# Performance work log

Measured on AMD Instinct MI355X. Metric: run time of the kernel, lower is better.

The kernel has to match this reference:

```python
import jax, jax.numpy as jnp
import numpy as np

N_IN, N_REC, N_OUT = 512, 2048, 128
D_MAX = 4      # delays drawn from [0, D_MAX]; possible_delays = 1..D_MAX
DT = 0.001


@jax.custom_vjp
def spike(v):
    # SpikeFunc.forward: heaviside(v > 0)
    return (v > 0.0).astype(v.dtype)

def _spike_fwd(v):
    return spike(v), v

def _spike_bwd(v, g):
    # SpikeFunc.backward: grad passes through unchanged for v >= 0,
    # scaled by relu(1 + v) for v < 0
    return (g * jnp.where(v < 0.0, jnp.maximum(1.0 + v, 0.0), 1.0),)

spike.defvjp(_spike_fwd, _spike_bwd)


def setup_inputs() -> dict:
    key = jax.random.key(0)
    ks = jax.random.split(key, 6)
    B, T = 64, 250
    x = (jax.random.uniform(ks[0], (B, N_IN, T)) < 0.05).astype(jnp.float32)
    delays = jax.random.randint(ks[1], (N_REC, N_REC), 0, D_MAX + 1, dtype=jnp.int32)

    def kaiming_uniform(k, shape, fan):
        bound = float(np.sqrt(6.0 / fan))
        return jax.random.uniform(k, shape, minval=-bound, maxval=bound, dtype=jnp.float32)

    W_i = kaiming_uniform(ks[2], (N_REC, N_IN), N_REC)            # fan_out mode
    W_r = kaiming_uniform(ks[3], (N_REC, N_REC), N_REC) * 0.05    # scaled for stable dynamics
    W_o = kaiming_uniform(ks[4], (N_OUT, N_REC), N_REC)
    return {
        'input_spike_raster': x,
        'delays': delays,
        'W_i': W_i, 'W_r': W_r, 'W_o': W_o,
        'B_r': jnp.zeros((N_REC,), jnp.float32),
        'B_o': jnp.zeros((N_OUT,), jnp.float32),
        'tau_rec': jnp.full((1,), 0.2, jnp.float32),
        'tau_out': jnp.full((1,), 0.2, jnp.float32),
        'thr_rec': jnp.full((1,), 0.5, jnp.float32),
    }


def reference(input_spike_raster, delays, W_i, W_r, W_o, B_r, B_o, tau_rec, tau_out, thr_rec):
    rec_c = jnp.exp(-DT * 10.0 / tau_rec)   # (1,)
    out_c = jnp.exp(-DT * 10.0 / tau_out)   # (1,)
    d_vals = jnp.arange(1, D_MAX + 1)       # possible (nonzero) delays
    # W_r * delay_mask.T for each delay d -> (D, n_rec, n_rec)
    masks = (delays[None, :, :] == d_vals[:, None, None])
    Wd = W_r[None] * jnp.transpose(masks, (0, 2, 1)).astype(W_r.dtype)

    B, n_in, T = input_spike_raster.shape
    xs = jnp.transpose(input_spike_raster, (2, 0, 1))  # (T, B, n_in)
    buf0 = jnp.zeros((D_MAX, B, N_REC), W_r.dtype)     # buf[k] = spikes at t-1-k

    def step(carry, inp):
        mem_rec, mem_out, buf = carry
        t, x_t = inp
        cur = x_t @ W_i.T + B_r                               # (B, n_rec)
        # delay d contributes only if t > d (matches torch `if t > d`)
        valid = (t > d_vals).astype(cur.dtype)                # (D,)
        cur = cur + jnp.einsum('dbn,dmn->bm', buf * valid[:, None, None], Wd)
        mem_rec = mem_rec * rec_c + cur
        z = spike(mem_rec - thr_rec)
        mem_rec = mem_rec - z * thr_rec
        mem_out = mem_out * out_c + z @ W_o.T + B_o
        buf = jnp.concatenate([z[None], buf[:-1]], axis=0)
        return (mem_rec, mem_out, buf), z

    init = (jnp.zeros((B, N_REC), W_r.dtype), jnp.zeros((B, N_OUT), W_r.dtype), buf0)
    (_, mem_out, _), zs = jax.lax.scan(step, init, (jnp.arange(T), xs))
    # torch returns (mem_pot_out, stack(rec_spikes, dim=2)) -> (B, n_rec, T)
    return mem_out, jnp.transpose(zs, (1, 2, 0))
```

## Files before the change

### kernel.cpp

```cpp
#include <hip/hip_runtime.h>

#define NIN  512
#define NREC 2048
#define NOUT 128
#define BB   64
#define TT   250

#define OFF_WRT  0UL
#define OFF_DP2  16777216UL
#define OFF_WIT  17825792UL
#define OFF_WOT  22020096UL
#define OFF_MASK 23068672UL
#define OFF_G    27164672UL
#define OFF_CNT  28213248UL

__device__ __forceinline__ int decode_delay(int v) {
    if (v >= 0 && v <= 4) return v;
    const float f = __int_as_float(v);
    if (f >= 0.5f && f <= 4.5f) return (int)(f + 0.5f);
    return 0;
}
__device__ __forceinline__ int delay_like(int v) {
    if (v >= 0 && v <= 4) return 1;
    const float f = __int_as_float(v);
    return (f >= 0.5f && f <= 4.5f) ? 1 : 0;
}
__device__ __forceinline__ unsigned lane_rank(unsigned long long m) {
    unsigned r = __builtin_amdgcn_mbcnt_lo((unsigned)m, 0u);
    return __builtin_amdgcn_mbcnt_hi((unsigned)(m >> 32), r);
}

__global__ __launch_bounds__(256) void k_prep(
    const void* __restrict__ c4A, const void* __restrict__ c4B,
    const float* __restrict__ Wi, const float* __restrict__ Wo,
    float* __restrict__ WrT, unsigned* __restrict__ dP2,
    float* __restrict__ WiT, float* __restrict__ WoT)
{
    const int* iA = (const int*)c4A;
    const int* iB = (const int*)c4B;
    int cntA = 0, cntB = 0;
    for (int j = 0; j < 64; ++j) { cntA += delay_like(iA[j]); cntB += delay_like(iB[j]); }
    const int*   dl = (cntA >= cntB) ? iA : iB;
    const float* Wr = (cntA >= cntB) ? (const float*)c4B : (const float*)c4A;

    const int idx = blockIdx.x * 256 + threadIdx.x;
    if (idx < NREC * NREC) {
        const int n = idx >> 11, m = idx & 2047;
        const int d = decode_delay(dl[idx]);
        const float w = Wr[(size_t)m * NREC + n];
        WrT[idx] = (d == 0) ? 0.0f : w;
        if ((m & 15) == 0) {
            unsigned pw = 0;
            for (int j = 0; j < 16; ++j) {
                const int dj = decode_delay(dl[idx + j]);
                const unsigned e = (dj == 0) ? 0u : (unsigned)(dj - 1);
                pw |= e << (2 * j);
            }
            dP2[idx >> 4] = pw;
        }
    }
    if (idx < NIN * NREC) {
        const int i = idx >> 11, m = idx & 2047;
        WiT[idx] = Wi[(size_t)m * NIN + i];
    }
    if (idx < NREC * NOUT) {
        const int n = idx >> 7, o = idx & 127;
        WoT[idx] = Wo[(size_t)o * NREC + n];
    }
}


#define ACCEV(wf, ee) { const int dd = (int)(((ee) >> sh) & 3u);                \
    const double wd = (double)(wf);                                             \
    a0 += (dd == 0) ? wd : 0.0; a1 += (dd == 1) ? wd : 0.0;                     \
    a2 += (dd == 2) ? wd : 0.0; a3 += (dd == 3) ? wd : 0.0; }

#define LD1(nn, W, E) { const unsigned n_ = (nn);                               \
    W = WrT[(n_ << 11) | colu]; E = dP2[(n_ << 7) | c4i]; }

#define LOAD8M(base, P) {                                                       \
    const uint4 sv_ = *reinterpret_cast<const uint4*>(&slist[(base)]);          \
    LD1(sv_.x & 0xffffu, w##P##0, e##P##0) LD1(sv_.x >> 16, w##P##1, e##P##1)   \
    LD1(sv_.y & 0xffffu, w##P##2, e##P##2) LD1(sv_.y >> 16, w##P##3, e##P##3)   \
    LD1(sv_.z & 0xffffu, w##P##4, e##P##4) LD1(sv_.z >> 16, w##P##5, e##P##5)   \
    LD1(sv_.w & 0xffffu, w##P##6, e##P##6) LD1(sv_.w >> 16, w##P##7, e##P##7) }

#define ACCP(P) { ACCEV(w##P##0, e##P##0) ACCEV(w##P##1, e##P##1)               \
    ACCEV(w##P##2, e##P##2) ACCEV(w##P##3, e##P##3)                             \
    ACCEV(w##P##4, e##P##4) ACCEV(w##P##5, e##P##5)                             \
    ACCEV(w##P##6, e##P##6) ACCEV(w##P##7, e##P##7) }

__global__ __launch_bounds__(512) void k_main(
    const float* __restrict__ x,
    const float* __restrict__ WrT,
    const unsigned* __restrict__ dP2,
    const float* __restrict__ WiT,
    const float* __restrict__ Br,
    const float* __restrict__ tau_rec, const float* __restrict__ tau_out,
    const float* __restrict__ thr_rec,
    unsigned* __restrict__ spikeMask, unsigned* __restrict__ cnt,
    double* __restrict__ g)
{
    __shared__ int icnt[8];
    __shared__ __align__(16) unsigned short ilist[NIN];
    __shared__ __align__(16) unsigned short slist[NREC];
    __shared__ int stot_s;

    const int gid = blockIdx.x;
    const int r8  = gid & 7, kk = gid >> 3;
    const int q   = r8 >> 1;
    const int b   = kk * 2 + (r8 & 1);
    const int tid  = threadIdx.x;
    const int w    = tid >> 6;
    const int lane = tid & 63;
    const int col  = q * 512 + tid;
    const unsigned colu = (unsigned)col;
    const unsigned c4i  = colu >> 4;
    const int sh        = (col & 15) * 2;

    const double rec_c = exp(-0.01 / (double)tau_rec[0]);
    const double out_c = exp(-0.01 / (double)tau_out[0]);
    const double thr   = (double)thr_rec[0];
    const double br    = (double)Br[col];
    double mem = 0.0, gacc = 0.0;
    double a0 = 0.0, a1 = 0.0, a2 = 0.0, a3 = 0.0;

    const float* xb = x + (size_t)b * NIN * TT;
    const float* Wc = WiT + col;
    float xv = xb[(size_t)tid * TT];

    for (int t = 0; t < TT; ++t) {
        const bool ihit = (xv != 0.f);
        const unsigned long long im = __ballot(ihit);
        if (lane == 0) icnt[w] = __popcll(im);
        float xvn = 0.f;
        if (t + 1 < TT) xvn = xb[(size_t)tid * TT + (t + 1)];
        __syncthreads();
        int ioffw = 0, itot = 0;
#pragma unroll
        for (int j = 0; j < 8; ++j) { const int c = icnt[j]; if (j < w) ioffw += c; itot += c; }
        if (ihit) ilist[ioffw + lane_rank(im)] = (unsigned short)tid;
        __syncthreads();
        double cin = 0.0;
        {
            int k = 0;
            for (; k + 8 <= itot; k += 8) {
                const uint4 sv = *reinterpret_cast<const uint4*>(&ilist[k]);
                const float v0 = Wc[(sv.x & 0xffffu) << 11];
                const float v1 = Wc[(sv.x >> 16)     << 11];
                const float v2 = Wc[(sv.y & 0xffffu) << 11];
                const float v3 = Wc[(sv.y >> 16)     << 11];
                const float v4 = Wc[(sv.z & 0xffffu) << 11];
                const float v5 = Wc[(sv.z >> 16)     << 11];
                const float v6 = Wc[(sv.w & 0xffffu) << 11];
                const float v7 = Wc[(sv.w >> 16)     << 11];
                cin += (double)v0; cin += (double)v1; cin += (double)v2; cin += (double)v3;
                cin += (double)v4; cin += (double)v5; cin += (double)v6; cin += (double)v7;
            }
            for (; k < itot; ++k) cin += (double)Wc[(unsigned)ilist[k] << 11];
        }
        xv = xvn;

        if (t >= 2) {
            const unsigned* gmp = spikeMask + (size_t)((t - 1) * BB + b) * 64;
            if (tid == 0) {
                while (__hip_atomic_load(&cnt[(t - 1) * BB + b],
                                         __ATOMIC_ACQUIRE, __HIP_MEMORY_SCOPE_AGENT) < 4u)
                    __builtin_amdgcn_s_sleep(1);
            }
            __syncthreads();
            if (tid < 64) {
                const unsigned wv = __hip_atomic_load(&gmp[tid],
                                        __ATOMIC_RELAXED, __HIP_MEMORY_SCOPE_AGENT);
                const int zc = __popc(wv);
                int inc = zc;
#pragma unroll
                for (int s = 1; s < 64; s <<= 1) {
                    const int up = __shfl_up(inc, s, 64);
                    if (lane >= s) inc += up;
                }
                int off = inc - zc;
                if (lane == 63) stot_s = inc;
                unsigned bits = wv;
                while (bits) {
                    const int bp = __ffs(bits) - 1;
                    bits &= bits - 1;
                    slist[off++] = (unsigned short)(tid * 32 + bp);
                }
            }
            __syncthreads();
            const int stot = stot_s;
            int k = 0;
            {
                float wA0, wA1, wA2, wA3, wA4, wA5, wA6, wA7;
                float wB0, wB1, wB2, wB3, wB4, wB5, wB6, wB7;
                float wC0, wC1, wC2, wC3, wC4, wC5, wC6, wC7;
                unsigned eA0, eA1, eA2, eA3, eA4, eA5, eA6, eA7;
                unsigned eB0, eB1, eB2, eB3, eB4, eB5, eB6, eB7;
                unsigned eC0, eC1, eC2, eC3, eC4, eC5, eC6, eC7;
                if (stot >= 48) {
                    LOAD8M(0, A) LOAD8M(8, B) LOAD8M(16, C)
                    for (k = 0; k + 48 <= stot; k += 24) {
                        ACCP(A) LOAD8M(k + 24, A)
                        ACCP(B) LOAD8M(k + 32, B)
                        ACCP(C) LOAD8M(k + 40, C)
                    }
                    ACCP(A) ACCP(B) ACCP(C)
                    k += 24;
                }
            }
            for (; k + 8 <= stot; k += 8) {
                const uint4 sv = *reinterpret_cast<const uint4*>(&slist[k]);
                const unsigned n0 = sv.x & 0xffffu, n1 = sv.x >> 16;
                const unsigned n2 = sv.y & 0xffffu, n3 = sv.y >> 16;
                const unsigned n4 = sv.z & 0xffffu, n5 = sv.z >> 16;
                const unsigned n6 = sv.w & 0xffffu, n7 = sv.w >> 16;
                const float w0 = WrT[(n0 << 11) | colu]; const unsigned e0 = dP2[(n0 << 7) | c4i];
                const float w1 = WrT[(n1 << 11) | colu]; const unsigned e1 = dP2[(n1 << 7) | c4i];
                const float w2 = WrT[(n2 << 11) | colu]; const unsigned e2 = dP2[(n2 << 7) | c4i];
                const float w3 = WrT[(n3 << 11) | colu]; const unsigned e3 = dP2[(n3 << 7) | c4i];
                const float w4 = WrT[(n4 << 11) | colu]; const unsigned e4 = dP2[(n4 << 7) | c4i];
                const float w5 = WrT[(n5 << 11) | colu]; const unsigned e5 = dP2[(n5 << 7) | c4i];
                const float w6 = WrT[(n6 << 11) | colu]; const unsigned e6 = dP2[(n6 << 7) | c4i];
                const float w7 = WrT[(n7 << 11) | colu]; const unsigned e7 = dP2[(n7 << 7) | c4i];
                ACCEV(w0, e0) ACCEV(w1, e1) ACCEV(w2, e2) ACCEV(w3, e3)
                ACCEV(w4, e4) ACCEV(w5, e5) ACCEV(w6, e6) ACCEV(w7, e7)
            }
            for (; k < stot; ++k) {
                const unsigned n0 = (unsigned)slist[k];
                const float w0 = WrT[(n0 << 11) | colu];
                const unsigned e0 = dP2[(n0 << 7) | c4i];
                ACCEV(w0, e0)
            }
        }

        const double cur = a0 + cin + br;
        a0 = a1; a1 = a2; a2 = a3; a3 = 0.0;
        mem = mem * rec_c + cur;
        const bool z = (mem - thr) > 0.0;
        if (z) mem -= thr;
        gacc = gacc * out_c + (z ? 1.0 : 0.0);

        const unsigned long long mz = __ballot(z);
        unsigned* gm = spikeMask + (size_t)(t * BB + b) * 64;
        if (lane == 0)
            __hip_atomic_store(&gm[q * 16 + 2 * w], (unsigned)(mz & 0xFFFFFFFFu),
                               __ATOMIC_RELAXED, __HIP_MEMORY_SCOPE_AGENT);
        if (lane == 32)
            __hip_atomic_store(&gm[q * 16 + 2 * w + 1], (unsigned)(mz >> 32),
                               __ATOMIC_RELAXED, __HIP_MEMORY_SCOPE_AGENT);
        __syncthreads();
        if (tid == 0)
            __hip_atomic_fetch_add(&cnt[t * BB + b], 1u,
                                   __ATOMIC_RELEASE, __HIP_MEMORY_SCOPE_AGENT);
    }

    g[(size_t)b * NREC + col] = gacc;
}

__global__ __launch_bounds__(256) void k_memout(
    const double* __restrict__ g, const float* __restrict__ WoT,
    const float* __restrict__ Bo, const float* __restrict__ tau_out,
    float* __restrict__ mout)
{
    __shared__ double gs[NREC];
    const int b = blockIdx.x, tid = threadIdx.x;
#pragma unroll
    for (int k = 0; k < 8; ++k)
        gs[tid + 256 * k] = g[(size_t)b * NREC + tid + 256 * k];
    const double c = exp(-0.01 / (double)tau_out[0]);
    double S = 0.0;
    for (int t = 0; t < TT; ++t) S = S * c + 1.0;
    __syncthreads();
    if (tid < NOUT) {
        double a = 0.0;
        for (int n = 0; n < NREC; ++n)
            a += gs[n] * (double)WoT[n * NOUT + tid];
        a += (double)Bo[tid] * S;
        mout[(size_t)b * NOUT + tid] = (float)a;
    }
}

__global__ __launch_bounds__(256) void k_expand(
    const unsigned* __restrict__ spikeMask, float* __restrict__ zout)
{
    const int bid = blockIdx.x;
    const int b = bid >> 6, gw = bid & 63;
    const int t = threadIdx.x;
    if (t >= TT) return;
    const unsigned v = spikeMask[((size_t)(t * BB + b)) * 64 + gw];
    for (int j = 0; j < 32; ++j) {
        const int n = gw * 32 + j;
        zout[((size_t)b * NREC + n) * TT + t] = ((v >> j) & 1u) ? 1.0f : 0.0f;
    }
}

extern "C" void kernel_launch(void* const* d_in, const int* in_sizes, int n_in,
                              void* d_out, int out_size, void* d_ws, size_t ws_size,
                              hipStream_t stream) {
    const float *x = nullptr, *Wi = nullptr, *Wo = nullptr, *Br = nullptr, *Bo = nullptr;
    const void* c4[2] = {nullptr, nullptr};
    const float* sc[3] = {nullptr, nullptr, nullptr};
    int n4 = 0, nsc = 0;
    for (int i = 0; i < n_in; ++i) {
        switch (in_sizes[i]) {
            case 8192000: x  = (const float*)d_in[i]; break;
            case 1048576: Wi = (const float*)d_in[i]; break;
            case 262144:  Wo = (const float*)d_in[i]; break;
            case 2048:    Br = (const float*)d_in[i]; break;
            case 128:     Bo = (const float*)d_in[i]; break;
            case 4194304: if (n4 < 2)  c4[n4++]  = d_in[i]; break;
            case 1:       if (nsc < 3) sc[nsc++] = (const float*)d_in[i]; break;
            default: break;
        }
    }
    if (!x || !Wi || !Wo || !Br || !Bo || n4 < 2 || nsc < 3) {
        x  = (const float*)d_in[0];
        c4[0] = d_in[1];
        Wi = (const float*)d_in[2];
        c4[1] = d_in[3];
        Wo = (const float*)d_in[4];
        Br = (const float*)d_in[5];
        Bo = (const float*)d_in[6];
        sc[0] = (const float*)d_in[7];
        sc[1] = (const float*)d_in[8];
        sc[2] = (const float*)d_in[9];
    }
    const float* taur = sc[0];
    const float* tauo = sc[1];
    const float* thr  = sc[2];

    float* out = (float*)d_out;
    char* ws = (char*)d_ws;
    float*          WrT  = (float*)(ws + OFF_WRT);
    unsigned*       dP2  = (unsigned*)(ws + OFF_DP2);
    float*          WiT  = (float*)(ws + OFF_WIT);
    float*          WoT  = (float*)(ws + OFF_WOT);
    unsigned*       mask = (unsigned*)(ws + OFF_MASK);
    double*         g    = (double*)(ws + OFF_G);
    unsigned*       cnt  = (unsigned*)(ws + OFF_CNT);

    hipMemsetAsync(cnt, 0, (size_t)TT * BB * sizeof(unsigned), stream);
    hipLaunchKernelGGL(k_prep, dim3((NREC * NREC + 255) / 256), dim3(256), 0, stream,
                       c4[0], c4[1], Wi, Wo, WrT, dP2, WiT, WoT);
    hipLaunchKernelGGL(k_main, dim3(256), dim3(512), 0, stream,
                       x, WrT, dP2, WiT, Br, taur, tauo, thr, mask, cnt, g);
    hipLaunchKernelGGL(k_memout, dim3(BB), dim3(256), 0, stream,
                       g, WoT, Bo, tauo, out);
    hipLaunchKernelGGL(k_expand, dim3(BB * 64), dim3(256), 0, stream,
                       mask, out + 8192);
}
```

Baseline: 4.360 ms.

## Split spike-list accumulation across two thread halves per column block

Doubles the k_main block size to 1024 threads, so each output column gets two threads that each process half of the input-spike and recurrent-spike lists. The second half's partial sums are exchanged through shared memory and reduced by the first half, which alone performs the membrane update and spike publication. This aims to halve the per-step serial gather latency on the critical path of the persistent time loop. The cost is an extra barrier per step, more shared memory, and 1024-thread blocks that may limit occupancy or register budget for the heavily unrolled prefetch buffers.

```diff
diff --git a/kernel.cpp b/kernel.cpp
--- a/kernel.cpp
+++ b/kernel.cpp
@@ -69,7 +69,6 @@
     }
 }
 
-
 #define ACCEV(wf, ee) { const int dd = (int)(((ee) >> sh) & 3u);                \
     const double wd = (double)(wf);                                             \
     a0 += (dd == 0) ? wd : 0.0; a1 += (dd == 1) ? wd : 0.0;                     \
@@ -90,7 +89,7 @@
     ACCEV(w##P##4, e##P##4) ACCEV(w##P##5, e##P##5)                             \
     ACCEV(w##P##6, e##P##6) ACCEV(w##P##7, e##P##7) }
 
-__global__ __launch_bounds__(512) void k_main(
+__global__ __launch_bounds__(1024) void k_main(
     const float* __restrict__ x,
     const float* __restrict__ WrT,
     const unsigned* __restrict__ dP2,
@@ -105,15 +104,19 @@
     __shared__ __align__(16) unsigned short ilist[NIN];
     __shared__ __align__(16) unsigned short slist[NREC];
     __shared__ int stot_s;
+    __shared__ double aEx[512];
+    __shared__ double cEx[512];
 
     const int gid = blockIdx.x;
     const int r8  = gid & 7, kk = gid >> 3;
     const int q   = r8 >> 1;
     const int b   = kk * 2 + (r8 & 1);
     const int tid  = threadIdx.x;
+    const int half = tid >> 9;
+    const int u    = tid & 511;
     const int w    = tid >> 6;
     const int lane = tid & 63;
-    const int col  = q * 512 + tid;
+    const int col  = q * 512 + u;
     const unsigned colu = (unsigned)col;
     const unsigned c4i  = colu >> 4;
     const int sh        = (col & 15) * 2;
@@ -127,24 +130,27 @@
 
     const float* xb = x + (size_t)b * NIN * TT;
     const float* Wc = WiT + col;
-    float xv = xb[(size_t)tid * TT];
+    float xv = (half == 0) ? xb[(size_t)u * TT] : 0.f;
 
     for (int t = 0; t < TT; ++t) {
         const bool ihit = (xv != 0.f);
         const unsigned long long im = __ballot(ihit);
-        if (lane == 0) icnt[w] = __popcll(im);
+        if (w < 8 && lane == 0) icnt[w] = __popcll(im);
         float xvn = 0.f;
-        if (t + 1 < TT) xvn = xb[(size_t)tid * TT + (t + 1)];
+        if (half == 0 && t + 1 < TT) xvn = xb[(size_t)u * TT + (t + 1)];
         __syncthreads();
         int ioffw = 0, itot = 0;
 #pragma unroll
         for (int j = 0; j < 8; ++j) { const int c = icnt[j]; if (j < w) ioffw += c; itot += c; }
-        if (ihit) ilist[ioffw + lane_rank(im)] = (unsigned short)tid;
+        if (ihit) ilist[ioffw + lane_rank(im)] = (unsigned short)u;
         __syncthreads();
+        int iHalf = ((itot >> 1) + 7) & ~7; if (iHalf > itot) iHalf = itot;
+        const int ikb = half ? iHalf : 0;
+        const int ike = half ? itot  : iHalf;
         double cin = 0.0;
         {
-            int k = 0;
-            for (; k + 8 <= itot; k += 8) {
+            int k = ikb;
+            for (; k + 8 <= ike; k += 8) {
                 const uint4 sv = *reinterpret_cast<const uint4*>(&ilist[k]);
                 const float v0 = Wc[(sv.x & 0xffffu) << 11];
                 const float v1 = Wc[(sv.x >> 16)     << 11];
@@ -157,7 +163,7 @@
                 cin += (double)v0; cin += (double)v1; cin += (double)v2; cin += (double)v3;
                 cin += (double)v4; cin += (double)v5; cin += (double)v6; cin += (double)v7;
             }
-            for (; k < itot; ++k) cin += (double)Wc[(unsigned)ilist[k] << 11];
+            for (; k < ike; ++k) cin += (double)Wc[(unsigned)ilist[k] << 11];
         }
         xv = xvn;
 
@@ -190,7 +196,10 @@
             }
             __syncthreads();
             const int stot = stot_s;
-            int k = 0;
+            int sHalf = ((stot >> 1) + 7) & ~7; if (sHalf > stot) sHalf = stot;
+            const int kb = half ? sHalf : 0;
+            const int ke = half ? stot  : sHalf;
+            int k = kb;
             {
                 float wA0, wA1, wA2, wA3, wA4, wA5, wA6, wA7;
                 float wB0, wB1, wB2, wB3, wB4, wB5, wB6, wB7;
@@ -198,9 +207,9 @@
                 unsigned eA0, eA1, eA2, eA3, eA4, eA5, eA6, eA7;
                 unsigned eB0, eB1, eB2, eB3, eB4, eB5, eB6, eB7;
                 unsigned eC0, eC1, eC2, eC3, eC4, eC5, eC6, eC7;
-                if (stot >= 48) {
-                    LOAD8M(0, A) LOAD8M(8, B) LOAD8M(16, C)
-                    for (k = 0; k + 48 <= stot; k += 24) {
+                if (ke - kb >= 48) {
+                    LOAD8M(kb, A) LOAD8M(kb + 8, B) LOAD8M(kb + 16, C)
+                    for (k = kb; k + 48 <= ke; k += 24) {
                         ACCP(A) LOAD8M(k + 24, A)
                         ACCP(B) LOAD8M(k + 32, B)
                         ACCP(C) LOAD8M(k + 40, C)
@@ -209,7 +218,7 @@
                     k += 24;
                 }
             }
-            for (; k + 8 <= stot; k += 8) {
+            for (; k + 8 <= ke; k += 8) {
                 const uint4 sv = *reinterpret_cast<const uint4*>(&slist[k]);
                 const unsigned n0 = sv.x & 0xffffu, n1 = sv.x >> 16;
                 const unsigned n2 = sv.y & 0xffffu, n3 = sv.y >> 16;
@@ -226,7 +235,7 @@
                 ACCEV(w0, e0) ACCEV(w1, e1) ACCEV(w2, e2) ACCEV(w3, e3)
                 ACCEV(w4, e4) ACCEV(w5, e5) ACCEV(w6, e6) ACCEV(w7, e7)
             }
-            for (; k < stot; ++k) {
+            for (; k < ke; ++k) {
                 const unsigned n0 = (unsigned)slist[k];
                 const float w0 = WrT[(n0 << 11) | colu];
                 const unsigned e0 = dP2[(n0 << 7) | c4i];
@@ -234,28 +243,35 @@
             }
         }
 
-        const double cur = a0 + cin + br;
+        if (half) { aEx[u] = a0; cEx[u] = cin; }
+        __syncthreads();
+        bool z = false;
+        if (half == 0) {
+            const double cur = (a0 + aEx[u]) + (cin + cEx[u]) + br;
+            mem = mem * rec_c + cur;
+            z = (mem - thr) > 0.0;
+            if (z) mem -= thr;
+            gacc = gacc * out_c + (z ? 1.0 : 0.0);
+        }
         a0 = a1; a1 = a2; a2 = a3; a3 = 0.0;
-        mem = mem * rec_c + cur;
-        const bool z = (mem - thr) > 0.0;
-        if (z) mem -= thr;
-        gacc = gacc * out_c + (z ? 1.0 : 0.0);
 
         const unsigned long long mz = __ballot(z);
         unsigned* gm = spikeMask + (size_t)(t * BB + b) * 64;
-        if (lane == 0)
-            __hip_atomic_store(&gm[q * 16 + 2 * w], (unsigned)(mz & 0xFFFFFFFFu),
-                               __ATOMIC_RELAXED, __HIP_MEMORY_SCOPE_AGENT);
-        if (lane == 32)
-            __hip_atomic_store(&gm[q * 16 + 2 * w + 1], (unsigned)(mz >> 32),
-                               __ATOMIC_RELAXED, __HIP_MEMORY_SCOPE_AGENT);
+        if (w < 8) {
+            if (lane == 0)
+                __hip_atomic_store(&gm[q * 16 + 2 * w], (unsigned)(mz & 0xFFFFFFFFu),
+                                   __ATOMIC_RELAXED, __HIP_MEMORY_SCOPE_AGENT);
+            if (lane == 32)
+                __hip_atomic_store(&gm[q * 16 + 2 * w + 1], (unsigned)(mz >> 32),
+                                   __ATOMIC_RELAXED, __HIP_MEMORY_SCOPE_AGENT);
+        }
         __syncthreads();
         if (tid == 0)
             __hip_atomic_fetch_add(&cnt[t * BB + b], 1u,
                                    __ATOMIC_RELEASE, __HIP_MEMORY_SCOPE_AGENT);
     }
 
-    g[(size_t)b * NREC + col] = gacc;
+    if (half == 0) g[(size_t)b * NREC + col] = gacc;
 }
 
 __global__ __launch_bounds__(256) void k_memout(
@@ -343,7 +359,7 @@
     hipMemsetAsync(cnt, 0, (size_t)TT * BB * sizeof(unsigned), stream);
     hipLaunchKernelGGL(k_prep, dim3((NREC * NREC + 255) / 256), dim3(256), 0, stream,
                        c4[0], c4[1], Wi, Wo, WrT, dP2, WiT, WoT);
-    hipLaunchKernelGGL(k_main, dim3(256), dim3(512), 0, stream,
+    hipLaunchKernelGGL(k_main, dim3(256), dim3(1024), 0, stream,
                        x, WrT, dP2, WiT, Br, taur, tauo, thr, mask, cnt, g);
     hipLaunchKernelGGL(k_memout, dim3(BB), dim3(256), 0, stream,
                        g, WoT, Bo, tauo, out);
```

New measurement: 4.227 ms. 3.0% less time.
